# Kernel optimization log

Measured on AMD Instinct MI355X. Metric: run time of the kernel, lower is better.

The kernel has to match this reference:

```python
import jax, jax.numpy as jnp
import numpy as np

B, S, D, H = 2, 2048, 1024, 16
DK = D // H


def setup_inputs() -> dict:
    key = jax.random.key(0)
    ks = jax.random.split(key, 8)
    std = 0.02
    inp = {
        "query": jax.random.normal(ks[0], (B, S, D), jnp.float32),
        "key": jax.random.normal(ks[1], (B, S, D), jnp.float32),
        "value": jax.random.normal(ks[2], (B, S, D), jnp.float32),
        # causal mask, 1 = attend, 0 = masked (matches masked_fill(mask==0, -1e9))
        "mask": jnp.broadcast_to(
            jnp.tril(jnp.ones((S, S), jnp.int32))[None, None], (B, 1, S, S)
        ),
        "wq_w": jax.random.normal(ks[3], (D, D), jnp.float32) * std,
        "wq_b": jnp.zeros((D,), jnp.float32),
        "wk_w": jax.random.normal(ks[4], (D, D), jnp.float32) * std,
        "wk_b": jnp.zeros((D,), jnp.float32),
        "wv_w": jax.random.normal(ks[5], (D, D), jnp.float32) * std,
        "wv_b": jnp.zeros((D,), jnp.float32),
        "wo_w": jax.random.normal(ks[6], (D, D), jnp.float32) * std,
        "wo_b": jnp.zeros((D,), jnp.float32),
    }
    return inp


def _split_heads(x, b):
    # [B, S, D] -> [B, H, S, DK]
    return x.reshape(b, -1, H, DK).transpose(0, 2, 1, 3)


def reference(query, key, value, mask, wq_w, wq_b, wk_w, wk_b, wv_w, wv_b, wo_w, wo_b):
    b = query.shape[0]
    q = _split_heads(query @ wq_w.T + wq_b, b)
    k = _split_heads(key @ wk_w.T + wk_b, b)
    v = _split_heads(value @ wv_w.T + wv_b, b)

    scale = 1.0 / np.sqrt(DK).astype(np.float32)
    scores = jnp.einsum("bhqd,bhkd->bhqk", q, k) * scale  # [B,H,Sq,Sk]
    scores = jnp.where(mask == 0, jnp.float32(-1e9), scores)
    attn = jax.nn.softmax(scores, axis=-1)  # dropout p=0 (eval)

    ctx = jnp.einsum("bhqk,bhkd->bhqd", attn, v)  # [B,H,Sq,DK]
    ctx = ctx.transpose(0, 2, 1, 3).reshape(b, -1, D)  # [B,Sq,D]
    out = ctx @ wo_w.T + wo_b
    return out, attn
```

## Files before the change

### kernel.cpp

```cpp
#include <hip/hip_runtime.h>
#include <hip/hip_bf16.h>

#define B_ 2
#define S_ 2048
#define D_ 1024
#define H_ 16
#define DK_ 64

typedef __attribute__((ext_vector_type(8))) short bf16x8;
typedef __attribute__((ext_vector_type(4))) float f32x4;

#define MFMA16(a, b, c) __builtin_amdgcn_mfma_f32_16x16x32_bf16((a), (b), (c), 0, 0, 0)

__device__ __forceinline__ unsigned short f2bf(float f) {
  __hip_bfloat16 h = __float2bfloat16(f);
  return *reinterpret_cast<unsigned short*>(&h);
}

__device__ __forceinline__ void gload_lds16(const void* g, void* l) {
  __builtin_amdgcn_global_load_lds((const __attribute__((address_space(1))) void*)g,
                                   (__attribute__((address_space(3))) void*)l, 16, 0, 0);
}

__global__ __launch_bounds__(256) void cvt_all(
    const float* __restrict__ s0, const float* __restrict__ s1, const float* __restrict__ s2,
    const float* __restrict__ s3, const float* __restrict__ s4, const float* __restrict__ s5,
    const float* __restrict__ s6,
    unsigned short* __restrict__ d0, unsigned short* __restrict__ d1,
    unsigned short* __restrict__ d2, unsigned short* __restrict__ d3,
    unsigned short* __restrict__ d4, unsigned short* __restrict__ d5,
    unsigned short* __restrict__ d6, int nbig, int nsmall) {
  const float* src; unsigned short* dst; int n4;
  switch (blockIdx.y) {
    case 0: src = s0; dst = d0; n4 = nbig; break;
    case 1: src = s1; dst = d1; n4 = nbig; break;
    case 2: src = s2; dst = d2; n4 = nbig; break;
    case 3: src = s3; dst = d3; n4 = nsmall; break;
    case 4: src = s4; dst = d4; n4 = nsmall; break;
    case 5: src = s5; dst = d5; n4 = nsmall; break;
    default: src = s6; dst = d6; n4 = nsmall; break;
  }
  int i = blockIdx.x * blockDim.x + threadIdx.x;
  int stride = gridDim.x * blockDim.x;
  for (; i < n4; i += stride) {
    float4 v = ((const float4*)src)[i];
    ushort4 o;
    o.x = f2bf(v.x); o.y = f2bf(v.y); o.z = f2bf(v.z); o.w = f2bf(v.w);
    ((ushort4*)dst)[i] = o;
  }
}

__device__ __forceinline__ void gemm_body(const unsigned short* __restrict__ A,
                                          const unsigned short* __restrict__ W,
                                          const float* __restrict__ bias,
                                          void* __restrict__ out,
                                          int mode, float scale, int tm, int tn) {
  __shared__ __align__(16) unsigned short lsA[128 * 32];
  __shared__ __align__(16) unsigned short lsB[128 * 32];
  const int K = 1024;
  const int tid = threadIdx.x;
  const int w = tid >> 6, l = tid & 63;
  const int wm = w >> 2, wn = w & 3;
  const int cl = l & 15, lg = l >> 4;

  f32x4 acc[4][2];
#pragma unroll
  for (int i = 0; i < 4; ++i)
#pragma unroll
    for (int j = 0; j < 2; ++j) acc[i][j] = (f32x4){0.f, 0.f, 0.f, 0.f};

  const int srow = w * 16 + (l >> 2);
  const int slog = (l & 3) ^ ((srow >> 1) & 3);
  const unsigned short* Abase = A + (size_t)(tm * 128 + srow) * K + slog * 8;
  const unsigned short* Wbase = W + (size_t)(tn * 128 + srow) * K + slog * 8;
  unsigned short* ldA = lsA + w * 512;
  unsigned short* ldB = lsB + w * 512;

  for (int ks = 0; ks < 32; ++ks) {
    const int k0 = ks * 32;
    gload_lds16(Abase + k0, ldA);
    gload_lds16(Wbase + k0, ldB);
    __syncthreads();

    bf16x8 af[4], bfr[2];
#pragma unroll
    for (int f = 0; f < 4; ++f) {
      int ar = wm * 64 + f * 16 + cl;
      int ph = lg ^ ((ar >> 1) & 3);
      af[f] = *(const bf16x8*)(lsA + ar * 32 + ph * 8);
    }
#pragma unroll
    for (int f = 0; f < 2; ++f) {
      int br = wn * 32 + f * 16 + cl;
      int ph = lg ^ ((br >> 1) & 3);
      bfr[f] = *(const bf16x8*)(lsB + br * 32 + ph * 8);
    }
#pragma unroll
    for (int i = 0; i < 4; ++i)
#pragma unroll
      for (int j = 0; j < 2; ++j) acc[i][j] = MFMA16(af[i], bfr[j], acc[i][j]);
    __syncthreads();
  }

#pragma unroll
  for (int i = 0; i < 4; ++i) {
#pragma unroll
    for (int j = 0; j < 2; ++j) {
#pragma unroll
      for (int r = 0; r < 4; ++r) {
        int mm = tm * 128 + wm * 64 + i * 16 + 4 * lg + r;
        int nn = tn * 128 + wn * 32 + j * 16 + cl;
        float v = (acc[i][j][r] + bias[nn]) * scale;
        if (mode == 2) {
          ((float*)out)[(size_t)mm * 1024 + nn] = v;
        } else {
          int bb = mm >> 11, s = mm & 2047, hh = nn >> 6, dk = nn & 63;
          size_t idx = (mode == 0)
                           ? ((((size_t)bb * H_ + hh) * S_ + s) * DK_ + dk)
                           : ((((size_t)bb * H_ + hh) * DK_ + dk) * S_ + s);
          ((unsigned short*)out)[idx] = f2bf(v);
        }
      }
    }
  }
}

#define QSCALE 0.18033688011112042f

__global__ __launch_bounds__(512) void gemm_qkv(
    const unsigned short* __restrict__ xq, const unsigned short* __restrict__ xk,
    const unsigned short* __restrict__ xv, const unsigned short* __restrict__ wq,
    const unsigned short* __restrict__ wk, const unsigned short* __restrict__ wv,
    const float* __restrict__ bq, const float* __restrict__ bk, const float* __restrict__ bv,
    unsigned short* __restrict__ oq, unsigned short* __restrict__ ok,
    unsigned short* __restrict__ ov) {
  const int z = blockIdx.z;
  const unsigned short* A = (z == 0) ? xq : (z == 1) ? xk : xv;
  const unsigned short* W = (z == 0) ? wq : (z == 1) ? wk : wv;
  const float* bias = (z == 0) ? bq : (z == 1) ? bk : bv;
  void* out = (z == 0) ? (void*)oq : (z == 1) ? (void*)ok : (void*)ov;
  gemm_body(A, W, bias, out, (z == 2) ? 1 : 0, (z == 0) ? QSCALE : 1.0f,
            blockIdx.x, blockIdx.y);
}

__global__ __launch_bounds__(512) void gemm_out(const unsigned short* __restrict__ A,
                                                const unsigned short* __restrict__ W,
                                                const float* __restrict__ bias,
                                                float* __restrict__ out) {
  gemm_body(A, W, bias, out, 2, 1.0f, blockIdx.x, blockIdx.y);
}

__global__ __launch_bounds__(256) void attn_fused(const unsigned short* __restrict__ qh,
                                                  const unsigned short* __restrict__ kh,
                                                  const unsigned short* __restrict__ vt,
                                                  float* __restrict__ attn,
                                                  unsigned short* __restrict__ ctxh) {
  __shared__ __align__(16) unsigned short kst[2][4096];
  __shared__ __align__(16) unsigned short vst[2][4096];
  __shared__ __align__(16) float pT[4][16 * 68];
  const int wgid = blockIdx.x;
  const int y = wgid >> 3;
  const int qt = 31 - (y >> 2);
  const int bh = (wgid & 7) * 4 + (y & 3);
  const int b = bh >> 4, h = bh & 15;
  const int w = threadIdx.x >> 6, l = threadIdx.x & 63;
  const int cl = l & 15, lg = l >> 4;
  const int qrb = qt * 64 + w * 16;
  const int qloc = w * 16 + cl;

  const unsigned short* kbh = kh + (size_t)bh * S_ * DK_;
  const unsigned short* vbh = vt + (size_t)bh * DK_ * S_;

  bf16x8 aq0, aq1;
  {
    const unsigned short* qp = qh + (size_t)bh * S_ * DK_ + (size_t)(qrb + cl) * DK_ + lg * 8;
    aq0 = *(const bf16x8*)qp;
    aq1 = *(const bf16x8*)(qp + 32);
  }

  const int sr0 = w * 16 + (l >> 3);
  const int sc = l & 7;
  auto stageK = [&](int kt, int buf) {
    const char* base = (const char*)kbh + (size_t)kt * 8192;
#pragma unroll
    for (int call = 0; call < 2; ++call) {
      int r = sr0 + call * 8;
      gload_lds16(base + r * 128 + ((sc ^ (r & 7)) << 4),
                  (char*)kst[buf] + w * 2048 + call * 1024);
    }
  };
  auto stageV = [&](int kt, int buf) {
    const char* base = (const char*)vbh + (size_t)kt * 128;
#pragma unroll
    for (int call = 0; call < 2; ++call) {
      int r = sr0 + call * 8;
      gload_lds16(base + (size_t)r * (S_ * 2) + ((sc ^ (r & 7)) << 4),
                  (char*)vst[buf] + w * 2048 + call * 1024);
    }
  };
  auto readK = [&](int buf, bf16x8(&k0)[4], bf16x8(&k1)[4]) {
#pragma unroll
    for (int mt = 0; mt < 4; ++mt) {
      int r = mt * 16 + cl;
      const char* rb = (const char*)kst[buf] + r * 128;
      k0[mt] = *(const bf16x8*)(rb + ((lg ^ (r & 7)) << 4));
      k1[mt] = *(const bf16x8*)(rb + (((4 + lg) ^ (r & 7)) << 4));
    }
  };

  f32x4 lsv = (f32x4){0.f, 0.f, 0.f, 0.f};
  stageK(0, 0);
  __syncthreads();
  for (int t = 0; t <= qt; ++t) {
    const int cur = t & 1;
    if (t < qt) stageK(t + 1, cur ^ 1);
    bf16x8 k0[4], k1[4];
    readK(cur, k0, k1);
    f32x4 cc[4];
#pragma unroll
    for (int mt = 0; mt < 4; ++mt) {
      f32x4 c = (f32x4){0.f, 0.f, 0.f, 0.f};
      c = MFMA16(k0[mt], aq0, c);
      cc[mt] = MFMA16(k1[mt], aq1, c);
    }
    const bool diag = (t == qt);
#pragma unroll
    for (int mt = 0; mt < 4; ++mt)
#pragma unroll
      for (int r = 0; r < 4; ++r) {
        float e = exp2f(cc[mt][r]);
        if (diag && (mt * 16 + 4 * lg + r > qloc)) e = 0.f;
        lsv[r] += e;
      }
    __syncthreads();
  }
  float ls = (lsv[0] + lsv[1]) + (lsv[2] + lsv[3]);
  ls += __shfl_xor(ls, 16);
  ls += __shfl_xor(ls, 32);
  const float inv = 1.0f / ls;

  f32x4 pv[4];
#pragma unroll
  for (int i = 0; i < 4; ++i) pv[i] = (f32x4){0.f, 0.f, 0.f, 0.f};
  float* pTw = pT[w];
  float* asrow = attn + (size_t)bh * S_ * S_ + (size_t)(qrb + lg) * S_ + 4 * cl;

  stageK(0, 0);
  stageV(0, 0);
  __syncthreads();
  for (int t = 0; t <= qt; ++t) {
    const int cur = t & 1;
    if (t < qt) {
      stageK(t + 1, cur ^ 1);
      stageV(t + 1, cur ^ 1);
    }
    bf16x8 k0[4], k1[4];
    readK(cur, k0, k1);
    f32x4 cc[4];
#pragma unroll
    for (int mt = 0; mt < 4; ++mt) {
      f32x4 c = (f32x4){0.f, 0.f, 0.f, 0.f};
      c = MFMA16(k0[mt], aq0, c);
      cc[mt] = MFMA16(k1[mt], aq1, c);
    }
    const bool diag = (t == qt);
#pragma unroll
    for (int mt = 0; mt < 4; ++mt) {
      f32x4 pf;
#pragma unroll
      for (int r = 0; r < 4; ++r) {
        float p = exp2f(cc[mt][r]) * inv;
        if (diag && (mt * 16 + 4 * lg + r > qloc)) p = 0.f;
        pf[r] = p;
      }
      *(f32x4*)(pTw + cl * 68 + mt * 16 + 4 * lg) = pf;
    }
#pragma unroll
    for (int j = 0; j < 4; ++j) {
      f32x4 v = *(const f32x4*)(pTw + (4 * j + lg) * 68 + 4 * cl);
      *(f32x4*)(asrow + (size_t)(4 * j) * S_ + t * 64) = v;
    }
#pragma unroll
    for (int c2 = 0; c2 < 2; ++c2) {
      f32x4 pa0 = *(const f32x4*)(pTw + cl * 68 + c2 * 32 + 8 * lg);
      f32x4 pa1 = *(const f32x4*)(pTw + cl * 68 + c2 * 32 + 8 * lg + 4);
      bf16x8 pa;
#pragma unroll
      for (int i = 0; i < 4; ++i) {
        pa[i] = (short)f2bf(pa0[i]);
        pa[4 + i] = (short)f2bf(pa1[i]);
      }
#pragma unroll
      for (int n2 = 0; n2 < 4; ++n2) {
        int r = n2 * 16 + cl;
        const char* rb = (const char*)vst[cur] + r * 128;
        bf16x8 vb = *(const bf16x8*)(rb + (((c2 * 4 + lg) ^ (r & 7)) << 4));
        pv[n2] = MFMA16(pa, vb, pv[n2]);
      }
    }
    __syncthreads();
  }

  {
    const f32x4 z = (f32x4){0.f, 0.f, 0.f, 0.f};
    for (int c = (qt + 1) * 64; c < S_; c += 64) {
#pragma unroll
      for (int j = 0; j < 4; ++j)
        *(f32x4*)(asrow + (size_t)(4 * j) * S_ + c) = z;
    }
  }

#pragma unroll
  for (int n2 = 0; n2 < 4; ++n2)
#pragma unroll
    for (int r = 0; r < 4; ++r)
      ctxh[((size_t)b * S_ + qrb + 4 * lg + r) * D_ + h * DK_ + n2 * 16 + cl] =
          f2bf(pv[n2][r]);
}

extern "C" void kernel_launch(void* const* d_in, const int* in_sizes, int n_in,
                              void* d_out, int out_size, void* d_ws, size_t ws_size,
                              hipStream_t stream) {
  const float* q  = (const float*)d_in[0];
  const float* k  = (const float*)d_in[1];
  const float* v  = (const float*)d_in[2];
  const float* wq = (const float*)d_in[4];
  const float* bq = (const float*)d_in[5];
  const float* wk = (const float*)d_in[6];
  const float* bk = (const float*)d_in[7];
  const float* wv = (const float*)d_in[8];
  const float* bv = (const float*)d_in[9];
  const float* wo = (const float*)d_in[10];
  const float* bo = (const float*)d_in[11];

  float* out  = (float*)d_out;
  float* attn = out + (size_t)B_ * S_ * D_;

  char* ws = (char*)d_ws;
  const size_t MB = 1024 * 1024;
  unsigned short* xq   = (unsigned short*)(ws + 0 * MB);
  unsigned short* xk   = (unsigned short*)(ws + 8 * MB);
  unsigned short* xv   = (unsigned short*)(ws + 16 * MB);
  unsigned short* wqb  = (unsigned short*)(ws + 24 * MB);
  unsigned short* wkb  = (unsigned short*)(ws + 26 * MB);
  unsigned short* wvb  = (unsigned short*)(ws + 28 * MB);
  unsigned short* wob  = (unsigned short*)(ws + 30 * MB);
  unsigned short* qhb  = (unsigned short*)(ws + 32 * MB);
  unsigned short* khb  = (unsigned short*)(ws + 40 * MB);
  unsigned short* vtb  = (unsigned short*)(ws + 48 * MB);
  unsigned short* ctxh = (unsigned short*)(ws + 56 * MB);

  const int NX4 = (B_ * S_ * D_) / 4;
  const int NW4 = (D_ * D_) / 4;
  cvt_all<<<dim3(256, 7), 256, 0, stream>>>(q, k, v, wq, wk, wv, wo,
                                            xq, xk, xv, wqb, wkb, wvb, wob, NX4, NW4);

  gemm_qkv<<<dim3(32, 8, 3), 512, 0, stream>>>(xq, xk, xv, wqb, wkb, wvb,
                                               bq, bk, bv, qhb, khb, vtb);

  attn_fused<<<dim3(1024), 256, 0, stream>>>(qhb, khb, vtb, attn, ctxh);

  gemm_out<<<dim3(32, 8), 512, 0, stream>>>(ctxh, wob, bo, out);
}
```

Measured before the change: 246.6 us.

## Double-buffer GEMM LDS tiles and use a four-buffer K ring in the softmax-sum pass

The projection GEMM now double-buffers its A and W LDS tiles. The next k-slice load is issued before computing on the current one, which removes one barrier per iteration and overlaps the global-to-LDS copy with MFMA work. The attention row-sum pass now handles two K tiles per iteration through a four-slot ring that reuses the V staging buffers. This prefetches two tiles ahead and halves the number of barriers. The cost is more LDS in the GEMM, which may lower occupancy, and extra code size from the unrolled pass.

```diff
diff --git a/kernel.cpp b/kernel.cpp
--- a/kernel.cpp
+++ b/kernel.cpp
@@ -55,8 +55,8 @@
                                           const float* __restrict__ bias,
                                           void* __restrict__ out,
                                           int mode, float scale, int tm, int tn) {
-  __shared__ __align__(16) unsigned short lsA[128 * 32];
-  __shared__ __align__(16) unsigned short lsB[128 * 32];
+  __shared__ __align__(16) unsigned short lsA[2][128 * 32];
+  __shared__ __align__(16) unsigned short lsB[2][128 * 32];
   const int K = 1024;
   const int tid = threadIdx.x;
   const int w = tid >> 6, l = tid & 63;
@@ -73,27 +73,29 @@
   const int slog = (l & 3) ^ ((srow >> 1) & 3);
   const unsigned short* Abase = A + (size_t)(tm * 128 + srow) * K + slog * 8;
   const unsigned short* Wbase = W + (size_t)(tn * 128 + srow) * K + slog * 8;
-  unsigned short* ldA = lsA + w * 512;
-  unsigned short* ldB = lsB + w * 512;
+
+  gload_lds16(Abase, lsA[0] + w * 512);
+  gload_lds16(Wbase, lsB[0] + w * 512);
+  __syncthreads();
 
   for (int ks = 0; ks < 32; ++ks) {
-    const int k0 = ks * 32;
-    gload_lds16(Abase + k0, ldA);
-    gload_lds16(Wbase + k0, ldB);
-    __syncthreads();
-
+    const int cur = ks & 1;
+    if (ks + 1 < 32) {
+      gload_lds16(Abase + (ks + 1) * 32, lsA[cur ^ 1] + w * 512);
+      gload_lds16(Wbase + (ks + 1) * 32, lsB[cur ^ 1] + w * 512);
+    }
     bf16x8 af[4], bfr[2];
 #pragma unroll
     for (int f = 0; f < 4; ++f) {
       int ar = wm * 64 + f * 16 + cl;
       int ph = lg ^ ((ar >> 1) & 3);
-      af[f] = *(const bf16x8*)(lsA + ar * 32 + ph * 8);
+      af[f] = *(const bf16x8*)(lsA[cur] + ar * 32 + ph * 8);
     }
 #pragma unroll
     for (int f = 0; f < 2; ++f) {
       int br = wn * 32 + f * 16 + cl;
       int ph = lg ^ ((br >> 1) & 3);
-      bfr[f] = *(const bf16x8*)(lsB + br * 32 + ph * 8);
+      bfr[f] = *(const bf16x8*)(lsB[cur] + br * 32 + ph * 8);
     }
 #pragma unroll
     for (int i = 0; i < 4; ++i)
@@ -180,13 +182,13 @@
 
   const int sr0 = w * 16 + (l >> 3);
   const int sc = l & 7;
-  auto stageK = [&](int kt, int buf) {
+  auto stageKp = [&](int kt, unsigned short* dst) {
     const char* base = (const char*)kbh + (size_t)kt * 8192;
 #pragma unroll
     for (int call = 0; call < 2; ++call) {
       int r = sr0 + call * 8;
       gload_lds16(base + r * 128 + ((sc ^ (r & 7)) << 4),
-                  (char*)kst[buf] + w * 2048 + call * 1024);
+                  (char*)dst + w * 2048 + call * 1024);
     }
   };
   auto stageV = [&](int kt, int buf) {
@@ -198,24 +200,21 @@
                   (char*)vst[buf] + w * 2048 + call * 1024);
     }
   };
-  auto readK = [&](int buf, bf16x8(&k0)[4], bf16x8(&k1)[4]) {
+  auto readKp = [&](const unsigned short* buf, bf16x8(&k0)[4], bf16x8(&k1)[4]) {
 #pragma unroll
     for (int mt = 0; mt < 4; ++mt) {
       int r = mt * 16 + cl;
-      const char* rb = (const char*)kst[buf] + r * 128;
+      const char* rb = (const char*)buf + r * 128;
       k0[mt] = *(const bf16x8*)(rb + ((lg ^ (r & 7)) << 4));
       k1[mt] = *(const bf16x8*)(rb + (((4 + lg) ^ (r & 7)) << 4));
     }
   };
+  auto kring = [&](int i) -> unsigned short* { return (i & 2) ? vst[i & 1] : kst[i & 1]; };
 
   f32x4 lsv = (f32x4){0.f, 0.f, 0.f, 0.f};
-  stageK(0, 0);
-  __syncthreads();
-  for (int t = 0; t <= qt; ++t) {
-    const int cur = t & 1;
-    if (t < qt) stageK(t + 1, cur ^ 1);
+  auto procA = [&](const unsigned short* buf, bool diag) {
     bf16x8 k0[4], k1[4];
-    readK(cur, k0, k1);
+    readKp(buf, k0, k1);
     f32x4 cc[4];
 #pragma unroll
     for (int mt = 0; mt < 4; ++mt) {
@@ -223,7 +222,6 @@
       c = MFMA16(k0[mt], aq0, c);
       cc[mt] = MFMA16(k1[mt], aq1, c);
     }
-    const bool diag = (t == qt);
 #pragma unroll
     for (int mt = 0; mt < 4; ++mt)
 #pragma unroll
@@ -232,6 +230,16 @@
         if (diag && (mt * 16 + 4 * lg + r > qloc)) e = 0.f;
         lsv[r] += e;
       }
+  };
+
+  stageKp(0, kring(0));
+  if (qt >= 1) stageKp(1, kring(1));
+  __syncthreads();
+  for (int t = 0; t <= qt; t += 2) {
+    if (t + 2 <= qt) stageKp(t + 2, kring(t + 2));
+    if (t + 3 <= qt) stageKp(t + 3, kring(t + 3));
+    procA(kring(t), t == qt);
+    if (t + 1 <= qt) procA(kring(t + 1), t + 1 == qt);
     __syncthreads();
   }
   float ls = (lsv[0] + lsv[1]) + (lsv[2] + lsv[3]);
@@ -245,17 +253,17 @@
   float* pTw = pT[w];
   float* asrow = attn + (size_t)bh * S_ * S_ + (size_t)(qrb + lg) * S_ + 4 * cl;
 
-  stageK(0, 0);
+  stageKp(0, kst[0]);
   stageV(0, 0);
   __syncthreads();
   for (int t = 0; t <= qt; ++t) {
     const int cur = t & 1;
     if (t < qt) {
-      stageK(t + 1, cur ^ 1);
+      stageKp(t + 1, kst[cur ^ 1]);
       stageV(t + 1, cur ^ 1);
     }
     bf16x8 k0[4], k1[4];
-    readK(cur, k0, k1);
+    readKp(kst[cur], k0, k1);
     f32x4 cc[4];
 #pragma unroll
     for (int mt = 0; mt < 4; ++mt) {
```

New measurement: 248.0 us. Within noise of the previous version (+0.6%).
